# Kernel tuning notes

Hardware: AMD Instinct MI355X
Metric: run time of the kernel (lower is better)

## Reference

```python
import jax, jax.numpy as jnp
import numpy as np

NODES_PER_GRAPH = 21
NUM_GRAPHS = 50000
N = NODES_PER_GRAPH * NUM_GRAPHS  # 1,050,000 nodes
NUM_FEATURES = 3
NUM_CLASSES = 29
H1, H2 = 64, 128
BN_EPS = 1e-5

_HAND = np.array([(0, 1), (1, 2), (2, 3), (3, 4), (0, 5), (5, 6), (6, 7), (7, 8),
                  (0, 9), (9, 10), (10, 11), (11, 12), (0, 13), (13, 14), (14, 15),
                  (15, 16), (0, 17), (17, 18), (18, 19), (19, 20)], dtype=np.int64).T  # [2,20]


def setup_inputs() -> dict:
    key = jax.random.key(0)
    ks = jax.random.split(key, 16)
    # Tile hand skeleton across NUM_GRAPHS disjoint graphs with node offsets.
    offsets = (np.arange(NUM_GRAPHS, dtype=np.int64) * NODES_PER_GRAPH)  # [G]
    ei = (_HAND[:, None, :] + offsets[None, :, None]).reshape(2, -1)      # [2, G*20]
    edge_index = jnp.asarray(ei)
    batch = jnp.asarray(np.repeat(np.arange(NUM_GRAPHS, dtype=np.int64), NODES_PER_GRAPH))

    x = jax.random.normal(ks[0], (N, NUM_FEATURES), dtype=jnp.float32)

    def lin(k, fi, fo):
        kw, kb = jax.random.split(k)
        s = 1.0 / np.sqrt(fi)
        return (jax.random.uniform(kw, (fi, fo), jnp.float32, -s, s),
                jax.random.uniform(kb, (fo,), jnp.float32, -s, s))

    W1, b1 = lin(ks[1], NUM_FEATURES, H1)
    W2, b2 = lin(ks[2], H1, H2)
    W3, b3 = lin(ks[3], H2, NUM_CLASSES)

    def bn(k, d):
        k1, k2, k3, k4 = jax.random.split(k, 4)
        return (1.0 + 0.1 * jax.random.normal(k1, (d,), jnp.float32),   # gamma
                0.1 * jax.random.normal(k2, (d,), jnp.float32),          # beta
                0.01 * jax.random.normal(k3, (d,), jnp.float32),         # running_mean
                jax.random.uniform(k4, (d,), jnp.float32, 0.5, 1.5))     # running_var

    g1, be1, m1, v1 = bn(ks[4], H1)
    g2, be2, m2, v2 = bn(ks[5], H2)

    return {"x": x, "W1": W1, "b1": b1, "g1": g1, "be1": be1, "m1": m1, "v1": v1,
            "W2": W2, "b2": b2, "g2": g2, "be2": be2, "m2": m2, "v2": v2,
            "W3": W3, "b3": b3, "edge_index": edge_index, "batch": batch}


def gcn_conv(x, W, b, src, dst):
    """PyG GCNConv: linear, add self-loops, sym-normalized scatter-add, bias."""
    h = x @ W                                              # [N, Fout]
    deg = jnp.zeros((N,), x.dtype).at[dst].add(1.0) + 1.0  # in-degree incl. self-loop
    dinv = deg ** -0.5
    msg = h[src] * (dinv[src] * dinv[dst])[:, None]        # edge-wise gather + normalize
    out = jnp.zeros_like(h).at[dst].add(msg)               # scatter-add aggregation
    out = out + h * (dinv * dinv)[:, None]                 # self-loop contribution
    return out + b


def bn_eval(x, gamma, beta, mean, var):
    return (x - mean) * (gamma * jax.lax.rsqrt(var + BN_EPS)) + beta


def reference(x, W1, b1, g1, be1, m1, v1, W2, b2, g2, be2, m2, v2, W3, b3,
              edge_index, batch):
    src, dst = edge_index[0], edge_index[1]
    h = jax.nn.relu(bn_eval(gcn_conv(x, W1, b1, src, dst), g1, be1, m1, v1))
    # dropout is identity in eval mode
    h = jax.nn.relu(bn_eval(gcn_conv(h, W2, b2, src, dst), g2, be2, m2, v2))
    h = gcn_conv(h, W3, b3, src, dst)                      # [N, C]
    summed = jax.ops.segment_sum(h, batch, num_segments=NUM_GRAPHS)
    counts = jax.ops.segment_sum(jnp.ones((N,), h.dtype), batch, num_segments=NUM_GRAPHS)
    pooled = summed / counts[:, None]                      # global mean pool [G, C]
    return jax.nn.log_softmax(pooled, axis=1)
```

## Files before the change

### kernel.cpp

```cpp
#include <hip/hip_runtime.h>
#include <math.h>


#define G_TOTAL 50000
#define GPB 4
#define CPB 5
#define NBLK (G_TOTAL / (GPB * CPB))
#define NCLS 29
#define BN_EPS 1e-5f
#define INV_SQRT2 0.70710678118654752440f
#define ROOT_W 0.21597780504441608f

#define WS_W1B  0
#define WS_B2   256
#define WS_B3   384
#define WS_W3T  416
#define WS_BF   4128
#define WS_TOTAL (WS_BF + 4096)

#define TSTRIDE 1056
#define FRAGBUF (12 * TSTRIDE)

typedef short s16x8 __attribute__((ext_vector_type(8)));
typedef float f32x4 __attribute__((ext_vector_type(4)));

__device__ __forceinline__ unsigned f2bf_rne(float f) {
    unsigned u = __float_as_uint(f);
    return (u + 0x7FFFu + ((u >> 16) & 1u)) >> 16;
}

__global__ void prep_kernel(const float* __restrict__ W1, const float* __restrict__ b1,
                            const float* __restrict__ g1, const float* __restrict__ be1,
                            const float* __restrict__ m1, const float* __restrict__ v1,
                            const float* __restrict__ W2, const float* __restrict__ b2,
                            const float* __restrict__ g2, const float* __restrict__ be2,
                            const float* __restrict__ m2, const float* __restrict__ v2,
                            const float* __restrict__ W3, const float* __restrict__ b3,
                            float* __restrict__ ws) {
    int t = blockIdx.x * blockDim.x + threadIdx.x;
    if (t < 256) {
        int k = t >> 2, comp = t & 3;
        float s = g1[k] * rsqrtf(v1[k] + BN_EPS);
        float v;
        if (comp < 3) v = W1[comp * 64 + k] * s;
        else          v = (b1[k] - m1[k]) * s + be1[k];
        ws[WS_W1B + t] = v;
    } else if (t < 384) {
        int j = t - 256;
        float s = g2[j] * rsqrtf(v2[j] + BN_EPS);
        ws[WS_B2 + j] = (b2[j] - m2[j]) * s + be2[j];
    } else if (t < 416) {
        int j = t - 384;
        ws[WS_B3 + j] = (j < NCLS) ? b3[j] : 0.f;
    } else if (t < WS_BF) {
        int i = t - WS_W3T;
        if (i < 3712) {
            int c = i >> 7, k = i & 127;
            ws[WS_W3T + i] = W3[k * NCLS + c];
        }
    } else if (t < WS_TOTAL) {
        int i = t - WS_BF;
        int d  = i & 3;
        int l  = (i >> 2) & 63;
        int ss = (i >> 8) & 1;
        int n  = i >> 9;
        int kg = l >> 4, r = l & 15;
        int c = 16 * n + r;
        float sc = g2[c] * rsqrtf(v2[c] + BN_EPS);
        int k0 = 32 * ss + 8 * kg + 2 * d;
        unsigned h0 = f2bf_rne(W2[k0 * 128 + c] * sc);
        unsigned h1 = f2bf_rne(W2[(k0 + 1) * 128 + c] * sc);
        ((unsigned*)ws)[WS_BF + i] = (h1 << 16) | h0;
    }
}

__global__ __launch_bounds__(256, 4)
void gcn_main(const float* __restrict__ x, const float* __restrict__ ws,
              float* __restrict__ out) {
    __shared__ __align__(16) char sFrag[2][FRAGBUF];
    __shared__ __align__(16) float4 sW1B[64];
    __shared__ __align__(16) float4 sX[2][64];
    __shared__ __align__(16) float sPool[4 * 132];

    const int tid = threadIdx.x;
    const int lane = tid & 63;
    const int w = tid >> 6;
    const int r = lane & 15;
    const int lg = lane >> 4;
    const long long cbase = (long long)blockIdx.x * CPB;

    const uint4* wsB = (const uint4*)((const unsigned*)ws + WS_BF);
    const uint4 B00 = wsB[((2*w+0)*2 + 0)*64 + lane];
    const uint4 B01 = wsB[((2*w+0)*2 + 1)*64 + lane];
    const uint4 B10 = wsB[((2*w+1)*2 + 0)*64 + lane];
    const uint4 B11 = wsB[((2*w+1)*2 + 1)*64 + lane];
    const float b2c0 = ws[WS_B2 + 32*w + r];
    const float b2c1 = ws[WS_B2 + 32*w + 16 + r];
    const int cc = lane >> 1;
    const int h3 = lane & 1;
    const float b3r = ws[WS_B3 + (cc < NCLS ? cc : 0)];
    const float* w3base = ws + WS_W3T + cc * 128 + 64 * h3;

    auto phase1 = [&](int buf) {
        if (tid < 168) {
            const int node = tid >> 1;
            const int s = tid & 1;
            const int k0q = s * 32;
            const int g4 = (node * 3121) >> 16;
            const int p  = node - 21 * g4;
            const int dist  = (p == 0) ? 0 : (((p & 3) == 1) ? p : 1);
            const float cw  = ((p & 3) == 1) ? INV_SQRT2 : 0.5f;
            const int jp = p - dist;
            const int dist2 = (jp == 0) ? 0 : (((jp & 3) == 1) ? jp : 1);
            const float cw2 = ((jp & 3) == 1) ? INV_SQRT2 : 0.5f;
            const float* xs = (const float*)&sX[buf][0] + node * 3;
            const float* xq = xs - dist * 3;
            const float* xg = xq - dist2 * 3;
            const float ax0 = fmaf(cw,  xq[0], 0.5f * xs[0]);
            const float ax1 = fmaf(cw,  xq[1], 0.5f * xs[1]);
            const float ax2 = fmaf(cw,  xq[2], 0.5f * xs[2]);
            const float bx0 = fmaf(cw2, xg[0], 0.5f * xq[0]);
            const float bx1 = fmaf(cw2, xg[1], 0.5f * xq[1]);
            const float bx2 = fmaf(cw2, xg[2], 0.5f * xq[2]);
            char* fragW = sFrag[buf] + ((p >> 2) * 2 + s) * TSTRIDE
                        + (4 * g4 + (p & 3)) * 16;
            #pragma unroll
            for (int q = 0; q < 4; ++q) {
                unsigned dws[4];
                #pragma unroll
                for (int pr = 0; pr < 4; ++pr) {
                    float azv[2];
                    #pragma unroll
                    for (int e = 0; e < 2; ++e) {
                        const float4 wv = sW1B[k0q + q*8 + pr*2 + e];
                        float ts = fmaf(ax0, wv.x, wv.w);
                        ts = fmaf(ax1, wv.y, ts);
                        ts = fmaf(ax2, wv.z, ts);
                        ts = fmaxf(ts, 0.f);
                        float tp = fmaf(bx0, wv.x, wv.w);
                        tp = fmaf(bx1, wv.y, tp);
                        tp = fmaf(bx2, wv.z, tp);
                        tp = fmaxf(tp, 0.f);
                        azv[e] = fmaf(cw, tp, 0.5f * ts);
                    }
                    dws[pr] = __builtin_amdgcn_perm(__float_as_uint(azv[1]),
                                                    __float_as_uint(azv[0]),
                                                    0x07060302u);
                }
                *(uint4*)(fragW + q * 256) =
                    make_uint4(dws[0], dws[1], dws[2], dws[3]);
            }
        }
    };

    if (tid < 64) sW1B[tid] = ((const float4*)ws)[tid];
    #pragma unroll
    for (int i = tid; i < 264; i += 256) {
        const int b = (i >= 132) ? 1 : 0;
        const int off = i - b * 132;
        *(float4*)(sFrag[b] + 10 * TSTRIDE + off * 16) =
            make_float4(0.f, 0.f, 0.f, 0.f);
    }
    float4 xr0, xr1, xreg;
    if (tid < 63) {
        xr0  = ((const float4*)(x + cbase * 252))[tid];
        xr1  = ((const float4*)(x + (cbase + 1) * 252))[tid];
        xreg = ((const float4*)(x + (cbase + 2) * 252))[tid];
        sX[0][tid] = xr0;
    }
    __syncthreads();
    phase1(0);
    if (tid < 63) sX[1][tid] = xr1;
    __syncthreads();

    for (int ck = 0; ck < CPB; ++ck) {
        const int cur = ck & 1;

        {
            const char* fragA = sFrag[cur] + lane * 16;
            float pg0 = 0.f, pg1 = 0.f;
            #pragma unroll
            for (int m = 0; m < 6; ++m) {
                const s16x8 A0 = *(const s16x8*)(fragA + (2*m + 0) * TSTRIDE);
                const s16x8 A1 = *(const s16x8*)(fragA + (2*m + 1) * TSTRIDE);
                f32x4 acc0 = {0.f, 0.f, 0.f, 0.f};
                f32x4 acc1 = {0.f, 0.f, 0.f, 0.f};
                acc0 = __builtin_amdgcn_mfma_f32_16x16x32_bf16(A0, *(const s16x8*)&B00, acc0, 0, 0, 0);
                acc0 = __builtin_amdgcn_mfma_f32_16x16x32_bf16(A1, *(const s16x8*)&B01, acc0, 0, 0, 0);
                acc1 = __builtin_amdgcn_mfma_f32_16x16x32_bf16(A0, *(const s16x8*)&B10, acc1, 0, 0, 0);
                acc1 = __builtin_amdgcn_mfma_f32_16x16x32_bf16(A1, *(const s16x8*)&B11, acc1, 0, 0, 0);
                #pragma unroll
                for (int i = 0; i < 4; ++i) {
                    const int p = 4*m + i;
                    if (p < 21) {
                        const float wgt = (p == 0) ? ROOT_W
                                        : (((p & 3) == 0) ? (0.5f / 21.f) : (1.f / 21.f));
                        pg0 = fmaf(wgt, fmaxf(acc0[i] + b2c0, 0.f), pg0);
                        pg1 = fmaf(wgt, fmaxf(acc1[i] + b2c1, 0.f), pg1);
                    }
                }
            }
            sPool[lg * 132 + 32*w + r]      = pg0;
            sPool[lg * 132 + 32*w + 16 + r] = pg1;

            if (ck < CPB - 1) phase1(cur ^ 1);
        }
        __syncthreads();

        {
            float v = -1e30f;
            if (lane < 2 * NCLS) {
                const float4* pp = (const float4*)&sPool[w * 132 + 64 * h3];
                const float4* w3 = (const float4*)w3base;
                float acc3 = 0.f;
                #pragma unroll
                for (int q = 0; q < 16; ++q) {
                    const float4 pv = pp[q];
                    const float4 wv = w3[q];
                    acc3 = fmaf(pv.x, wv.x, acc3);
                    acc3 = fmaf(pv.y, wv.y, acc3);
                    acc3 = fmaf(pv.z, wv.z, acc3);
                    acc3 = fmaf(pv.w, wv.w, acc3);
                }
                v = acc3;
            }
            v += __shfl_xor(v, 1);
            if (lane < 2 * NCLS) v += b3r;
            float m = v;
            m = fmaxf(m, __shfl_xor(m, 2));
            m = fmaxf(m, __shfl_xor(m, 4));
            m = fmaxf(m, __shfl_xor(m, 8));
            m = fmaxf(m, __shfl_xor(m, 16));
            m = fmaxf(m, __shfl_xor(m, 32));
            float e = (lane < 2 * NCLS) ? __expf(v - m) : 0.f;
            float ss = e;
            ss += __shfl_xor(ss, 2);
            ss += __shfl_xor(ss, 4);
            ss += __shfl_xor(ss, 8);
            ss += __shfl_xor(ss, 16);
            ss += __shfl_xor(ss, 32);
            if (h3 == 0 && lane < 2 * NCLS)
                out[((cbase + ck) * GPB + w) * NCLS + cc] = v - m - __logf(ss);

            if (tid < 63) {
                if (ck <= CPB - 3) sX[cur][tid] = xreg;
                if (ck <= CPB - 4)
                    xreg = ((const float4*)(x + (cbase + ck + 3) * 252))[tid];
            }
        }
        __syncthreads();
    }
}

extern "C" void kernel_launch(void* const* d_in, const int* in_sizes, int n_in,
                              void* d_out, int out_size, void* d_ws, size_t ws_size,
                              hipStream_t stream) {
    const float* x   = (const float*)d_in[0];
    const float* W1  = (const float*)d_in[1];
    const float* b1  = (const float*)d_in[2];
    const float* g1  = (const float*)d_in[3];
    const float* be1 = (const float*)d_in[4];
    const float* m1  = (const float*)d_in[5];
    const float* v1  = (const float*)d_in[6];
    const float* W2  = (const float*)d_in[7];
    const float* b2  = (const float*)d_in[8];
    const float* g2  = (const float*)d_in[9];
    const float* be2 = (const float*)d_in[10];
    const float* m2  = (const float*)d_in[11];
    const float* v2  = (const float*)d_in[12];
    const float* W3  = (const float*)d_in[13];
    const float* b3  = (const float*)d_in[14];
    float* out = (float*)d_out;
    float* ws  = (float*)d_ws;

    prep_kernel<<<(WS_TOTAL + 255) / 256, 256, 0, stream>>>(
        W1, b1, g1, be1, m1, v1, W2, b2, g2, be2, m2, v2, W3, b3, ws);

    gcn_main<<<NBLK, 256, 0, stream>>>(x, ws, out);
}
```

Before: 187.6 us.

## Shrink per-block chunks and single-buffer fragments to raise occupancy

Each block now processes 2 chunks instead of 5, so the grid is larger, and the fragment LDS buffer drops from double to single buffering. Launch bounds go from 4 to 8 blocks per CU. Phase-1 results for the next chunk are held in 16 registers during the MFMA pass and written to LDS after a barrier. The x loads are spread across different thread ranges and the loop is fully unrolled. The aim is more resident waves to hide latency, at the cost of more per-block setup work (B fragment loads, W1 staging) and more register pressure.

```diff
diff --git a/kernel.cpp b/kernel.cpp
--- a/kernel.cpp
+++ b/kernel.cpp
@@ -4,7 +4,7 @@
 
 #define G_TOTAL 50000
 #define GPB 4
-#define CPB 5
+#define CPB 2
 #define NBLK (G_TOTAL / (GPB * CPB))
 #define NCLS 29
 #define BN_EPS 1e-5f
@@ -19,7 +19,6 @@
 #define WS_TOTAL (WS_BF + 4096)
 
 #define TSTRIDE 1056
-#define FRAGBUF (12 * TSTRIDE)
 
 typedef short s16x8 __attribute__((ext_vector_type(8)));
 typedef float f32x4 __attribute__((ext_vector_type(4)));
@@ -74,10 +73,10 @@
     }
 }
 
-__global__ __launch_bounds__(256, 4)
+__global__ __launch_bounds__(256, 8)
 void gcn_main(const float* __restrict__ x, const float* __restrict__ ws,
               float* __restrict__ out) {
-    __shared__ __align__(16) char sFrag[2][FRAGBUF];
+    __shared__ __align__(16) char sFrag[12 * TSTRIDE];
     __shared__ __align__(16) float4 sW1B[64];
     __shared__ __align__(16) float4 sX[2][64];
     __shared__ __align__(16) float sPool[4 * 132];
@@ -88,6 +87,14 @@
     const int r = lane & 15;
     const int lg = lane >> 4;
     const long long cbase = (long long)blockIdx.x * CPB;
+
+    if (tid >= 192 && tid < 255)
+        sX[0][tid - 192] = ((const float4*)(x + cbase * 252))[tid - 192];
+    if (tid >= 128 && tid < 191)
+        sX[1][tid - 128] = ((const float4*)(x + (cbase + 1) * 252))[tid - 128];
+    if (tid < 64) sW1B[tid] = ((const float4*)ws)[tid];
+    if (tid < 132)
+        *(float4*)(sFrag + 10 * TSTRIDE + tid * 16) = make_float4(0.f, 0.f, 0.f, 0.f);
 
     const uint4* wsB = (const uint4*)((const unsigned*)ws + WS_BF);
     const uint4 B00 = wsB[((2*w+0)*2 + 0)*64 + lane];
@@ -101,155 +108,137 @@
     const float b3r = ws[WS_B3 + (cc < NCLS ? cc : 0)];
     const float* w3base = ws + WS_W3T + cc * 128 + 64 * h3;
 
-    auto phase1 = [&](int buf) {
-        if (tid < 168) {
-            const int node = tid >> 1;
-            const int s = tid & 1;
-            const int k0q = s * 32;
-            const int g4 = (node * 3121) >> 16;
-            const int p  = node - 21 * g4;
-            const int dist  = (p == 0) ? 0 : (((p & 3) == 1) ? p : 1);
-            const float cw  = ((p & 3) == 1) ? INV_SQRT2 : 0.5f;
-            const int jp = p - dist;
-            const int dist2 = (jp == 0) ? 0 : (((jp & 3) == 1) ? jp : 1);
-            const float cw2 = ((jp & 3) == 1) ? INV_SQRT2 : 0.5f;
-            const float* xs = (const float*)&sX[buf][0] + node * 3;
-            const float* xq = xs - dist * 3;
-            const float* xg = xq - dist2 * 3;
-            const float ax0 = fmaf(cw,  xq[0], 0.5f * xs[0]);
-            const float ax1 = fmaf(cw,  xq[1], 0.5f * xs[1]);
-            const float ax2 = fmaf(cw,  xq[2], 0.5f * xs[2]);
-            const float bx0 = fmaf(cw2, xg[0], 0.5f * xq[0]);
-            const float bx1 = fmaf(cw2, xg[1], 0.5f * xq[1]);
-            const float bx2 = fmaf(cw2, xg[2], 0.5f * xq[2]);
-            char* fragW = sFrag[buf] + ((p >> 2) * 2 + s) * TSTRIDE
-                        + (4 * g4 + (p & 3)) * 16;
+    const int node = tid >> 1;
+    const int s1v = tid & 1;
+    const int k0q = s1v * 32;
+    const int g4 = (node * 3121) >> 16;
+    const int p  = node - 21 * g4;
+    const int dist  = (p == 0) ? 0 : (((p & 3) == 1) ? p : 1);
+    const float cw  = ((p & 3) == 1) ? INV_SQRT2 : 0.5f;
+    const int jp = p - dist;
+    const int dist2 = (jp == 0) ? 0 : (((jp & 3) == 1) ? jp : 1);
+    const float cw2 = ((jp & 3) == 1) ? INV_SQRT2 : 0.5f;
+    const int xoff = node * 3;
+    char* const fragW = sFrag + ((p >> 2) * 2 + s1v) * TSTRIDE
+                      + (4 * g4 + (p & 3)) * 16;
+
+    unsigned dws[16];
+
+    auto p1_compute = [&](int buf) {
+        const float* xs = (const float*)&sX[buf][0] + xoff;
+        const float* xq = xs - dist * 3;
+        const float* xg = xq - dist2 * 3;
+        const float ax0 = fmaf(cw,  xq[0], 0.5f * xs[0]);
+        const float ax1 = fmaf(cw,  xq[1], 0.5f * xs[1]);
+        const float ax2 = fmaf(cw,  xq[2], 0.5f * xs[2]);
+        const float bx0 = fmaf(cw2, xg[0], 0.5f * xq[0]);
+        const float bx1 = fmaf(cw2, xg[1], 0.5f * xq[1]);
+        const float bx2 = fmaf(cw2, xg[2], 0.5f * xq[2]);
+        #pragma unroll
+        for (int q = 0; q < 16; ++q) {
+            float azv[2];
             #pragma unroll
-            for (int q = 0; q < 4; ++q) {
-                unsigned dws[4];
-                #pragma unroll
-                for (int pr = 0; pr < 4; ++pr) {
-                    float azv[2];
-                    #pragma unroll
-                    for (int e = 0; e < 2; ++e) {
-                        const float4 wv = sW1B[k0q + q*8 + pr*2 + e];
-                        float ts = fmaf(ax0, wv.x, wv.w);
-                        ts = fmaf(ax1, wv.y, ts);
-                        ts = fmaf(ax2, wv.z, ts);
-                        ts = fmaxf(ts, 0.f);
-                        float tp = fmaf(bx0, wv.x, wv.w);
-                        tp = fmaf(bx1, wv.y, tp);
-                        tp = fmaf(bx2, wv.z, tp);
-                        tp = fmaxf(tp, 0.f);
-                        azv[e] = fmaf(cw, tp, 0.5f * ts);
-                    }
-                    dws[pr] = __builtin_amdgcn_perm(__float_as_uint(azv[1]),
-                                                    __float_as_uint(azv[0]),
-                                                    0x07060302u);
-                }
-                *(uint4*)(fragW + q * 256) =
-                    make_uint4(dws[0], dws[1], dws[2], dws[3]);
+            for (int e = 0; e < 2; ++e) {
+                const float4 wv = sW1B[k0q + 2*q + e];
+                float ts = fmaf(ax0, wv.x, wv.w);
+                ts = fmaf(ax1, wv.y, ts);
+                ts = fmaf(ax2, wv.z, ts);
+                ts = fmaxf(ts, 0.f);
+                float tp = fmaf(bx0, wv.x, wv.w);
+                tp = fmaf(bx1, wv.y, tp);
+                tp = fmaf(bx2, wv.z, tp);
+                tp = fmaxf(tp, 0.f);
+                azv[e] = fmaf(cw, tp, 0.5f * ts);
             }
-        }
-    };
-
-    if (tid < 64) sW1B[tid] = ((const float4*)ws)[tid];
-    #pragma unroll
-    for (int i = tid; i < 264; i += 256) {
-        const int b = (i >= 132) ? 1 : 0;
-        const int off = i - b * 132;
-        *(float4*)(sFrag[b] + 10 * TSTRIDE + off * 16) =
-            make_float4(0.f, 0.f, 0.f, 0.f);
-    }
-    float4 xr0, xr1, xreg;
-    if (tid < 63) {
-        xr0  = ((const float4*)(x + cbase * 252))[tid];
-        xr1  = ((const float4*)(x + (cbase + 1) * 252))[tid];
-        xreg = ((const float4*)(x + (cbase + 2) * 252))[tid];
-        sX[0][tid] = xr0;
-    }
-    __syncthreads();
-    phase1(0);
-    if (tid < 63) sX[1][tid] = xr1;
-    __syncthreads();
-
-    for (int ck = 0; ck < CPB; ++ck) {
-        const int cur = ck & 1;
-
-        {
-            const char* fragA = sFrag[cur] + lane * 16;
-            float pg0 = 0.f, pg1 = 0.f;
+            dws[q] = __builtin_amdgcn_perm(__float_as_uint(azv[1]),
+                                           __float_as_uint(azv[0]), 0x07060302u);
+        }
+    };
+    auto p1_write = [&]() {
+        #pragma unroll
+        for (int q = 0; q < 4; ++q)
+            *(uint4*)(fragW + q * 256) =
+                make_uint4(dws[4*q], dws[4*q+1], dws[4*q+2], dws[4*q+3]);
+    };
+
+    auto mfma_pool = [&]() {
+        const char* fragA = sFrag + lane * 16;
+        float pg0 = 0.f, pg1 = 0.f;
+        #pragma unroll
+        for (int m = 0; m < 6; ++m) {
+            const s16x8 A0 = *(const s16x8*)(fragA + (2*m + 0) * TSTRIDE);
+            const s16x8 A1 = *(const s16x8*)(fragA + (2*m + 1) * TSTRIDE);
+            f32x4 acc0 = {0.f, 0.f, 0.f, 0.f};
+            f32x4 acc1 = {0.f, 0.f, 0.f, 0.f};
+            acc0 = __builtin_amdgcn_mfma_f32_16x16x32_bf16(A0, *(const s16x8*)&B00, acc0, 0, 0, 0);
+            acc0 = __builtin_amdgcn_mfma_f32_16x16x32_bf16(A1, *(const s16x8*)&B01, acc0, 0, 0, 0);
+            acc1 = __builtin_amdgcn_mfma_f32_16x16x32_bf16(A0, *(const s16x8*)&B10, acc1, 0, 0, 0);
+            acc1 = __builtin_amdgcn_mfma_f32_16x16x32_bf16(A1, *(const s16x8*)&B11, acc1, 0, 0, 0);
             #pragma unroll
-            for (int m = 0; m < 6; ++m) {
-                const s16x8 A0 = *(const s16x8*)(fragA + (2*m + 0) * TSTRIDE);
-                const s16x8 A1 = *(const s16x8*)(fragA + (2*m + 1) * TSTRIDE);
-                f32x4 acc0 = {0.f, 0.f, 0.f, 0.f};
-                f32x4 acc1 = {0.f, 0.f, 0.f, 0.f};
-                acc0 = __builtin_amdgcn_mfma_f32_16x16x32_bf16(A0, *(const s16x8*)&B00, acc0, 0, 0, 0);
-                acc0 = __builtin_amdgcn_mfma_f32_16x16x32_bf16(A1, *(const s16x8*)&B01, acc0, 0, 0, 0);
-                acc1 = __builtin_amdgcn_mfma_f32_16x16x32_bf16(A0, *(const s16x8*)&B10, acc1, 0, 0, 0);
-                acc1 = __builtin_amdgcn_mfma_f32_16x16x32_bf16(A1, *(const s16x8*)&B11, acc1, 0, 0, 0);
-                #pragma unroll
-                for (int i = 0; i < 4; ++i) {
-                    const int p = 4*m + i;
-                    if (p < 21) {
-                        const float wgt = (p == 0) ? ROOT_W
-                                        : (((p & 3) == 0) ? (0.5f / 21.f) : (1.f / 21.f));
-                        pg0 = fmaf(wgt, fmaxf(acc0[i] + b2c0, 0.f), pg0);
-                        pg1 = fmaf(wgt, fmaxf(acc1[i] + b2c1, 0.f), pg1);
-                    }
+            for (int i = 0; i < 4; ++i) {
+                const int pp = 4*m + i;
+                if (pp < 21) {
+                    const float wgt = (pp == 0) ? ROOT_W
+                                    : (((pp & 3) == 0) ? (0.5f / 21.f) : (1.f / 21.f));
+                    pg0 = fmaf(wgt, fmaxf(acc0[i] + b2c0, 0.f), pg0);
+                    pg1 = fmaf(wgt, fmaxf(acc1[i] + b2c1, 0.f), pg1);
                 }
             }
-            sPool[lg * 132 + 32*w + r]      = pg0;
-            sPool[lg * 132 + 32*w + 16 + r] = pg1;
-
-            if (ck < CPB - 1) phase1(cur ^ 1);
-        }
-        __syncthreads();
-
-        {
-            float v = -1e30f;
-            if (lane < 2 * NCLS) {
-                const float4* pp = (const float4*)&sPool[w * 132 + 64 * h3];
-                const float4* w3 = (const float4*)w3base;
-                float acc3 = 0.f;
-                #pragma unroll
-                for (int q = 0; q < 16; ++q) {
-                    const float4 pv = pp[q];
-                    const float4 wv = w3[q];
-                    acc3 = fmaf(pv.x, wv.x, acc3);
-                    acc3 = fmaf(pv.y, wv.y, acc3);
-                    acc3 = fmaf(pv.z, wv.z, acc3);
-                    acc3 = fmaf(pv.w, wv.w, acc3);
-                }
-                v = acc3;
+        }
+        sPool[lg * 132 + 32*w + r]      = pg0;
+        sPool[lg * 132 + 32*w + 16 + r] = pg1;
+    };
+
+    auto p3_out = [&](int ck) {
+        float v = -1e30f;
+        if (lane < 2 * NCLS) {
+            const float4* pp = (const float4*)&sPool[w * 132 + 64 * h3];
+            const float4* w3 = (const float4*)w3base;
+            float acc3 = 0.f;
+            #pragma unroll
+            for (int q = 0; q < 16; ++q) {
+                const float4 pv = pp[q];
+                const float4 wv = w3[q];
+                acc3 = fmaf(pv.x, wv.x, acc3);
+                acc3 = fmaf(pv.y, wv.y, acc3);
+                acc3 = fmaf(pv.z, wv.z, acc3);
+                acc3 = fmaf(pv.w, wv.w, acc3);
             }
-            v += __shfl_xor(v, 1);
-            if (lane < 2 * NCLS) v += b3r;
-            float m = v;
-            m = fmaxf(m, __shfl_xor(m, 2));
-            m = fmaxf(m, __shfl_xor(m, 4));
-            m = fmaxf(m, __shfl_xor(m, 8));
-            m = fmaxf(m, __shfl_xor(m, 16));
-            m = fmaxf(m, __shfl_xor(m, 32));
-            float e = (lane < 2 * NCLS) ? __expf(v - m) : 0.f;
-            float ss = e;
-            ss += __shfl_xor(ss, 2);
-            ss += __shfl_xor(ss, 4);
-            ss += __shfl_xor(ss, 8);
-            ss += __shfl_xor(ss, 16);
-            ss += __shfl_xor(ss, 32);
-            if (h3 == 0 && lane < 2 * NCLS)
-                out[((cbase + ck) * GPB + w) * NCLS + cc] = v - m - __logf(ss);
-
-            if (tid < 63) {
-                if (ck <= CPB - 3) sX[cur][tid] = xreg;
-                if (ck <= CPB - 4)
-                    xreg = ((const float4*)(x + (cbase + ck + 3) * 252))[tid];
-            }
-        }
-        __syncthreads();
-    }
+            v = acc3;
+        }
+        v += __shfl_xor(v, 1);
+        if (lane < 2 * NCLS) v += b3r;
+        float m = v;
+        m = fmaxf(m, __shfl_xor(m, 2));
+        m = fmaxf(m, __shfl_xor(m, 4));
+        m = fmaxf(m, __shfl_xor(m, 8));
+        m = fmaxf(m, __shfl_xor(m, 16));
+        m = fmaxf(m, __shfl_xor(m, 32));
+        float e = (lane < 2 * NCLS) ? __expf(v - m) : 0.f;
+        float ss = e;
+        ss += __shfl_xor(ss, 2);
+        ss += __shfl_xor(ss, 4);
+        ss += __shfl_xor(ss, 8);
+        ss += __shfl_xor(ss, 16);
+        ss += __shfl_xor(ss, 32);
+        if (h3 == 0 && lane < 2 * NCLS)
+            out[((cbase + ck) * GPB + w) * NCLS + cc] = v - m - __logf(ss);
+    };
+
+    __syncthreads();
+    if (tid < 168) { p1_compute(0); p1_write(); }
+    __syncthreads();
+
+    mfma_pool();
+    if (tid < 168) p1_compute(1);
+    __syncthreads();
+    if (tid < 168) p1_write();
+    p3_out(0);
+    __syncthreads();
+
+    mfma_pool();
+    __syncthreads();
+    p3_out(1);
 }
 
 extern "C" void kernel_launch(void* const* d_in, const int* in_sizes, int n_in,
```

New measurement: 334.5 us. 1.78x slower.
